# Kernel optimization log

Measured on AMD Instinct MI355X. Metric: run time of the kernel, lower is better.

## Reference

```python
import jax, jax.numpy as jnp
import numpy as np


def log_g(x):
    # Appendix B.3 of 'Were RNNs All We Needed?'
    return jnp.where(x >= 0, jnp.log(jax.nn.relu(x) + 0.5), -jax.nn.softplus(-x))


def parallel_scan_log(log_a, log_b):
    # h[0] = b[0]; h[i] = a[i]*h[i-1] + b[i], computed in log space along axis 1
    log_a_star = jnp.cumsum(log_a, axis=1)
    log_x0_plus_b_star = jax.lax.cumlogsumexp(log_b - log_a_star, axis=1)
    return jnp.exp(log_a_star + log_x0_plus_b_star)


def setup_inputs() -> dict:
    key = jax.random.key(0)
    B, T, D = 8, 4096, 1024
    k1, k2, k3, k4, k5 = jax.random.split(key, 5)
    scale = 1.0 / np.sqrt(D)
    return {
        "h_prev_layer": jax.random.normal(k1, (B, T, D), dtype=jnp.float32),
        "W_z": jax.random.uniform(k2, (D, D), jnp.float32, -scale, scale),
        "b_z": jax.random.uniform(k3, (D,), jnp.float32, -scale, scale),
        "W_h": jax.random.uniform(k4, (D, D), jnp.float32, -scale, scale),
        "b_h": jax.random.uniform(k5, (D,), jnp.float32, -scale, scale),
    }


def reference(h_prev_layer, W_z, b_z, W_h, b_h):
    k = jnp.einsum('btd,ed->bte', h_prev_layer, W_z) + b_z          # linear_z
    tilde_h = jnp.einsum('btd,ed->bte', h_prev_layer, W_h) + b_h    # linear_h
    log_z = -jax.nn.softplus(-k)
    log_one_minus_z = -jax.nn.softplus(k)
    log_tilde_h = log_g(tilde_h)
    return parallel_scan_log(log_one_minus_z, log_z + log_tilde_h)
```

## Files before the change

kernel.cpp:

```cpp
#include <hip/hip_runtime.h>
#include <hip/hip_fp16.h>

typedef float f32x4 __attribute__((ext_vector_type(4)));
typedef __bf16 bf16x8 __attribute__((ext_vector_type(8)));

#define BB_ 8
#define TT_ 4096
#define DD_ 1024
#define MM_ (BB_*TT_)
#define KK_ DD_

#define NCH 64
#define LCH (TT_/NCH)

static __device__ __forceinline__ unsigned short f2bf_rn(float f) {
  unsigned int u = __float_as_uint(f);
  u += 0x7FFFu + ((u >> 16) & 1u);
  return (unsigned short)(u >> 16);
}

__global__ void cvt_f32_bf16(const float4* __restrict__ src,
                             ushort4* __restrict__ dst, int n4) {
  int stride = gridDim.x * blockDim.x;
  for (int i = blockIdx.x * blockDim.x + threadIdx.x; i < n4; i += stride) {
    float4 v = src[i];
    ushort4 o;
    o.x = f2bf_rn(v.x); o.y = f2bf_rn(v.y);
    o.z = f2bf_rn(v.z); o.w = f2bf_rn(v.w);
    dst[i] = o;
  }
}

__global__ void cvt_w(const float4* __restrict__ Wz4,
                      const float4* __restrict__ Wh4,
                      ushort4* __restrict__ Wcat) {
  int flat = blockIdx.x * 256 + threadIdx.x;
  int mtx = flat >> 18;
  int j = flat & 262143;
  float4 v = (mtx ? Wh4 : Wz4)[j];
  int D = j >> 8;
  int kq = j & 255;
  int e = ((D >> 5) << 6) + (mtx << 5) + (D & 31);
  ushort4 o;
  o.x = f2bf_rn(v.x); o.y = f2bf_rn(v.y);
  o.z = f2bf_rn(v.z); o.w = f2bf_rn(v.w);
  Wcat[(size_t)e * 256 + kq] = o;
}

__device__ __forceinline__ void gload_lds16(const void* g, void* l) {
  __builtin_amdgcn_global_load_lds(
      (const __attribute__((address_space(1))) void*)g,
      (__attribute__((address_space(3))) void*)l, 16, 0, 0);
}

#define STA(q, nb_, kkh) gload_lds16(pXa + (q) * 65536 + (kkh), (nb_) + (q) * 8192 + wofs)
#define STB(q, nb_, kkh) gload_lds16(pWb + (q) * 65536 + (kkh), (nb_) + 32768 + (q) * 8192 + wofs)

#define PHASE(cb_, mh, kh, STAGEOPS, WAITOPS) do {                          \
    const char* Ab_ = (cb_);                                                \
    const char* Bb_ = (cb_) + 32768;                                        \
    const int sk_ = (kh) ? sk1 : sk0;                                       \
    bf16x8 af_[4];                                                          \
    _Pragma("unroll")                                                       \
    for (int ii = 0; ii < 4; ++ii)                                          \
      af_[ii] = *reinterpret_cast<const bf16x8*>(                           \
          Ab_ + rA7 + (mh) * 8192 + ii * 2048 + sk_);                       \
    if ((mh) == 0) {                                                        \
      _Pragma("unroll")                                                     \
      for (int j = 0; j < 4; ++j)                                           \
        bfv[j] = *reinterpret_cast<const bf16x8*>(                          \
            Bb_ + rB7 + j * 2048 + sk_);                                    \
    }                                                                       \
    STAGEOPS;                                                               \
    WAITOPS;                                                                \
    __builtin_amdgcn_s_barrier();                                           \
    asm volatile("s_waitcnt lgkmcnt(0)" ::: "memory");                      \
    __builtin_amdgcn_sched_barrier(0);                                      \
    __builtin_amdgcn_s_setprio(1);                                          \
    _Pragma("unroll")                                                       \
    for (int ii = 0; ii < 4; ++ii)                                          \
      _Pragma("unroll")                                                     \
      for (int j = 0; j < 4; ++j)                                           \
        acc[(mh) * 4 + ii][j] = __builtin_amdgcn_mfma_f32_16x16x32_bf16(    \
            af_[ii], bfv[j], acc[(mh) * 4 + ii][j], 0, 0, 0);               \
    __builtin_amdgcn_s_setprio(0);                                          \
    asm volatile("" ::: "memory");                                          \
    __builtin_amdgcn_s_barrier();                                           \
  } while (0)

__global__ __launch_bounds__(512, 2) void gemm_fused(
    const unsigned short* __restrict__ Xb,
    const unsigned short* __restrict__ Wb,
    const float* __restrict__ bz, const float* __restrict__ bh,
    unsigned int* __restrict__ ZG,
    float* __restrict__ Pp, float* __restrict__ Qq)
{
  extern __shared__ __align__(16) char smem[];
  const int tid  = threadIdx.x;
  const int wave = tid >> 6;
  const int lane = tid & 63;
  const int wm = wave >> 2, wn = wave & 3;
  const int fr = lane & 15, kg = lane >> 4;

  int swz = (blockIdx.x & 7) * 128 + (blockIdx.x >> 3);
  const int m0 = (swz >> 3) * 256;
  const int e0 = (swz & 7) * 256;

  const int arow = tid >> 3;
  const int aslx = ((tid & 7) ^ (arow & 7)) * 8;
  const unsigned short* pXa = Xb + (size_t)(m0 + arow) * KK_ + aslx;
  const unsigned short* pWb = Wb + (size_t)(e0 + arow) * KK_ + aslx;
  const int wofs = wave * 1024;

  const int rA7 = (wm * 128 + fr) * 128;
  const int rB7 = (wn * 64 + fr) * 128;
  const int fx = fr & 7;
  const int sk0 = (kg ^ fx) * 16;
  const int sk1 = sk0 ^ 64;

  f32x4 acc[8][4];
  #pragma unroll
  for (int i = 0; i < 8; i++)
    #pragma unroll
    for (int j = 0; j < 4; j++)
      acc[i][j] = (f32x4){0.f, 0.f, 0.f, 0.f};
  bf16x8 bfv[4];

  STA(0, smem, 0); STA(2, smem, 0); STB(0, smem, 0);
  STB(1, smem, 0); STB(2, smem, 0); STB(3, smem, 0);
  STA(1, smem, 0); STA(3, smem, 0);
  asm volatile("s_waitcnt vmcnt(2)" ::: "memory");
  __builtin_amdgcn_s_barrier();

  #pragma unroll 1
  for (int t = 0; t < 15; ++t) {
    char* cb = smem + ((t & 1) << 16);
    char* nb = smem + (((t + 1) & 1) << 16);
    const int kn = (t + 1) * 64;
    PHASE(cb, 0, 0, {STA(0, nb, kn); STA(2, nb, kn); STB(0, nb, kn);},
          asm volatile("s_waitcnt vmcnt(3)" ::: "memory"));
    PHASE(cb, 1, 0, {STB(1, nb, kn); STB(2, nb, kn); STB(3, nb, kn);}, );
    PHASE(cb, 0, 1, {STA(1, nb, kn); STA(3, nb, kn);}, );
    PHASE(cb, 1, 1, {},
          asm volatile("s_waitcnt vmcnt(2)" ::: "memory"));
  }
  {
    char* cb = smem + 65536;
    PHASE(cb, 0, 0, {}, asm volatile("s_waitcnt vmcnt(0)" ::: "memory"));
    PHASE(cb, 1, 0, {}, );
    PHASE(cb, 0, 1, {}, );
    PHASE(cb, 1, 1, {}, );
  }

  const int dw0 = (swz & 7) * 128 + wn * 32;
  const int t0 = m0 & 4095;
  const int bidx = m0 >> 12;

  float bzv[2], bhv[2];
  #pragma unroll
  for (int j = 0; j < 2; ++j) {
    bzv[j] = bz[dw0 + j * 16 + fr];
    bhv[j] = bh[dw0 + j * 16 + fr];
  }

  unsigned int* ew = (unsigned int*)(smem + wave * 9216);
  const int sub = lane & 7, rowr = lane >> 3;

  #pragma unroll
  for (int p = 0; p < 2; ++p) {
    float PP[2] = {1.f, 1.f}, QQ[2] = {0.f, 0.f};
    #pragma unroll
    for (int ii = 0; ii < 4; ++ii) {
      #pragma unroll
      for (int j = 0; j < 2; ++j) {
        float segP = 1.f, segQ = 0.f;
        #pragma unroll
        for (int r = 0; r < 4; ++r) {
          float kz = acc[p * 4 + ii][j][r] + bzv[j];
          float th = acc[p * 4 + ii][j + 2][r] + bhv[j];
          float z = 1.0f / (1.0f + __expf(-kz));
          float g = (th >= 0.0f) ? (th + 0.5f)
                                 : (1.0f / (1.0f + __expf(-th)));
          unsigned int pk =
              (unsigned int)__half_as_ushort(__float2half(z)) |
              ((unsigned int)__half_as_ushort(__float2half(g)) << 16);
          ew[(ii * 16 + kg * 4 + r) * 36 + j * 16 + fr] = pk;
          float aa = 1.f - z;
          segP *= aa;
          segQ = fmaf(aa, segQ, z * g);
        }
        float p1 = __shfl_down(segP, 16), q1 = __shfl_down(segQ, 16);
        segQ = fmaf(p1, segQ, q1); segP *= p1;
        float p2 = __shfl_down(segP, 32), q2 = __shfl_down(segQ, 32);
        segQ = fmaf(p2, segQ, q2); segP *= p2;
        QQ[j] = fmaf(segP, QQ[j], segQ);
        PP[j] *= segP;
      }
    }
    if (kg == 0) {
      const int cg = (t0 >> 6) + wm * 2 + p;
      #pragma unroll
      for (int j = 0; j < 2; ++j) {
        size_t po = ((size_t)bidx * NCH + cg) * DD_ + dw0 + j * 16 + fr;
        Pp[po] = PP[j];
        Qq[po] = QQ[j];
      }
    }
    #pragma unroll
    for (int q = 0; q < 8; ++q) {
      int rl = q * 8 + rowr;
      uint4 v = *reinterpret_cast<const uint4*>(&ew[rl * 36 + sub * 4]);
      size_t rg = (size_t)(m0 + wm * 128 + p * 64 + rl);
      *reinterpret_cast<uint4*>(&ZG[rg * DD_ + dw0 + sub * 4]) = v;
    }
  }
}

__global__ __launch_bounds__(256) void scan_combine(
    const float* __restrict__ P, const float* __restrict__ Q,
    float* __restrict__ H) {
  const int d = blockIdx.x * 256 + threadIdx.x;
  const int b = blockIdx.y;
  float h = 0.f;
  for (int c = 0; c < NCH; ++c) {
    size_t o = ((size_t)b * NCH + c) * DD_ + d;
    H[o] = h;
    h = fmaf(P[o], h, Q[o]);
  }
}

__global__ __launch_bounds__(256) void scan_apply(
    const uint4* __restrict__ ZG, const float4* __restrict__ H,
    float4* __restrict__ out) {
  const int d4 = threadIdx.x;
  const int c  = blockIdx.x;
  const int b  = blockIdx.y;
  float4 h = H[((size_t)b * NCH + c) * (DD_ / 4) + d4];
  size_t base = ((size_t)b * TT_ + (size_t)c * LCH) * (DD_ / 4) + d4;
  for (int t = 0; t < LCH; ++t) {
    uint4 w = ZG[base + (size_t)t * (DD_ / 4)];
    float z, g, a;
    z = __half2float(__ushort_as_half((unsigned short)(w.x & 0xffff)));
    g = __half2float(__ushort_as_half((unsigned short)(w.x >> 16)));
    a = 1.f - z; h.x = fmaf(a, h.x, z * g);
    z = __half2float(__ushort_as_half((unsigned short)(w.y & 0xffff)));
    g = __half2float(__ushort_as_half((unsigned short)(w.y >> 16)));
    a = 1.f - z; h.y = fmaf(a, h.y, z * g);
    z = __half2float(__ushort_as_half((unsigned short)(w.z & 0xffff)));
    g = __half2float(__ushort_as_half((unsigned short)(w.z >> 16)));
    a = 1.f - z; h.z = fmaf(a, h.z, z * g);
    z = __half2float(__ushort_as_half((unsigned short)(w.w & 0xffff)));
    g = __half2float(__ushort_as_half((unsigned short)(w.w >> 16)));
    a = 1.f - z; h.w = fmaf(a, h.w, z * g);
    out[base + (size_t)t * (DD_ / 4)] = h;
  }
}

extern "C" void kernel_launch(void* const* d_in, const int* in_sizes, int n_in,
                              void* d_out, int out_size, void* d_ws, size_t ws_size,
                              hipStream_t stream) {
  const float* X  = (const float*)d_in[0];
  const float* Wz = (const float*)d_in[1];
  const float* bz = (const float*)d_in[2];
  const float* Wh = (const float*)d_in[3];
  const float* bh = (const float*)d_in[4];
  float* out = (float*)d_out;

  const size_t szXb = (size_t)MM_ * DD_ * 2;
  const size_t szWb = (size_t)2 * DD_ * DD_ * 2;
  const size_t szZG = (size_t)MM_ * DD_ * 4;
  const size_t szPQ = (size_t)BB_ * NCH * DD_ * 4;

  char* ws = (char*)d_ws;
  unsigned short *Xb, *Wb;
  const size_t needA = szXb + szWb + szZG + 3 * szPQ;
  if (ws_size >= needA) {
    Xb = (unsigned short*)ws;              ws += szXb;
    Wb = (unsigned short*)ws;              ws += szWb;
  } else {
    Xb = (unsigned short*)d_out;
    Wb = (unsigned short*)((char*)d_out + szXb);
  }
  unsigned int* ZG = (unsigned int*)ws;  ws += szZG;
  float* P = (float*)ws;  ws += szPQ;
  float* Q = (float*)ws;  ws += szPQ;
  float* H = (float*)ws;

  cvt_f32_bf16<<<2048, 256, 0, stream>>>((const float4*)X, (ushort4*)Xb,
                                         (int)((size_t)MM_ * DD_ / 4));
  cvt_w<<<2048, 256, 0, stream>>>((const float4*)Wz, (const float4*)Wh,
                                  (ushort4*)Wb);
  gemm_fused<<<(MM_ / 256) * ((2 * DD_) / 256), 512, 131072, stream>>>(
      Xb, Wb, bz, bh, ZG, P, Q);

  scan_combine<<<dim3(4, BB_), 256, 0, stream>>>(P, Q, H);
  scan_apply<<<dim3(NCH, BB_), 256, 0, stream>>>((const uint4*)ZG,
                                                 (const float4*)H, (float4*)out);
}
```

Before: 264.1 us.

## Shrink GEMM tile to 128x256 with 4 waves and BK=32 double buffering

Restructures the fused GEMM from 256x256 tiles with 8 waves and K-step 64 (128 KB LDS) to 128x256 tiles with 4 waves, K-step 32 and 48 KB LDS. The LDS swizzle, staging layout and epilogue pass structure are reworked to match. The aim is more resident blocks per CU and better latency hiding. The cost is more K iterations, more barriers, and less data reuse per tile, which raises global traffic for the B matrix.

```diff
diff --git a/kernel.cpp b/kernel.cpp
--- a/kernel.cpp
+++ b/kernel.cpp
@@ -53,23 +53,20 @@
       (__attribute__((address_space(3))) void*)l, 16, 0, 0);
 }
 
-#define STA(q, nb_, kkh) gload_lds16(pXa + (q) * 65536 + (kkh), (nb_) + (q) * 8192 + wofs)
-#define STB(q, nb_, kkh) gload_lds16(pWb + (q) * 65536 + (kkh), (nb_) + 32768 + (q) * 8192 + wofs)
-
-#define PHASE(cb_, mh, kh, STAGEOPS, WAITOPS) do {                          \
-    const char* Ab_ = (cb_);                                                \
-    const char* Bb_ = (cb_) + 32768;                                        \
-    const int sk_ = (kh) ? sk1 : sk0;                                       \
+#define STA(q, nb_, kkh) gload_lds16(pXa + (q) * 65536 + (kkh), (nb_) + (q) * 4096 + wofs)
+#define STB(q, nb_, kkh) gload_lds16(pWb + (q) * 65536 + (kkh), (nb_) + 8192 + (q) * 4096 + wofs)
+
+#define PH(cb_, mh, STAGEOPS, WAITOPS) do {                                 \
+    const char* Ab_ = (const char*)(cb_);                                   \
     bf16x8 af_[4];                                                          \
     _Pragma("unroll")                                                       \
     for (int ii = 0; ii < 4; ++ii)                                          \
       af_[ii] = *reinterpret_cast<const bf16x8*>(                           \
-          Ab_ + rA7 + (mh) * 8192 + ii * 2048 + sk_);                       \
+          Ab_ + rAb + (mh) * 4096 + ii * 1024);                             \
     if ((mh) == 0) {                                                        \
       _Pragma("unroll")                                                     \
       for (int j = 0; j < 4; ++j)                                           \
-        bfv[j] = *reinterpret_cast<const bf16x8*>(                          \
-            Bb_ + rB7 + j * 2048 + sk_);                                    \
+        bfv[j] = *reinterpret_cast<const bf16x8*>(Ab_ + rBb + j * 1024);    \
     }                                                                       \
     STAGEOPS;                                                               \
     WAITOPS;                                                                \
@@ -88,7 +85,9 @@
     __builtin_amdgcn_s_barrier();                                           \
   } while (0)
 
-__global__ __launch_bounds__(512, 2) void gemm_fused(
+#define VMW(n) asm volatile("s_waitcnt vmcnt(" #n ")" ::: "memory")
+
+__global__ __launch_bounds__(256, 2) void gemm_fused(
     const unsigned short* __restrict__ Xb,
     const unsigned short* __restrict__ Wb,
     const float* __restrict__ bz, const float* __restrict__ bh,
@@ -99,24 +98,22 @@
   const int tid  = threadIdx.x;
   const int wave = tid >> 6;
   const int lane = tid & 63;
-  const int wm = wave >> 2, wn = wave & 3;
+  const int wn = wave;
   const int fr = lane & 15, kg = lane >> 4;
 
-  int swz = (blockIdx.x & 7) * 128 + (blockIdx.x >> 3);
-  const int m0 = (swz >> 3) * 256;
+  int swz = (blockIdx.x & 7) * 256 + (blockIdx.x >> 3);
+  const int m0 = (swz >> 3) * 128;
   const int e0 = (swz & 7) * 256;
 
-  const int arow = tid >> 3;
-  const int aslx = ((tid & 7) ^ (arow & 7)) * 8;
-  const unsigned short* pXa = Xb + (size_t)(m0 + arow) * KK_ + aslx;
-  const unsigned short* pWb = Wb + (size_t)(e0 + arow) * KK_ + aslx;
+  const int rr = tid >> 2;
+  const int ac = ((tid & 3) ^ (rr & 3)) * 8;
+  const unsigned short* pXa = Xb + (size_t)(m0 + rr) * KK_ + ac;
+  const unsigned short* pWb = Wb + (size_t)(e0 + rr) * KK_ + ac;
   const int wofs = wave * 1024;
 
-  const int rA7 = (wm * 128 + fr) * 128;
-  const int rB7 = (wn * 64 + fr) * 128;
-  const int fx = fr & 7;
-  const int sk0 = (kg ^ fx) * 16;
-  const int sk1 = sk0 ^ 64;
+  const int cksw = ((kg ^ (fr & 3)) << 4);
+  const int rAb = fr * 64 + cksw;
+  const int rBb = 8192 + (wn * 64 + fr) * 64 + cksw;
 
   f32x4 acc[8][4];
   #pragma unroll
@@ -126,30 +123,25 @@
       acc[i][j] = (f32x4){0.f, 0.f, 0.f, 0.f};
   bf16x8 bfv[4];
 
-  STA(0, smem, 0); STA(2, smem, 0); STB(0, smem, 0);
-  STB(1, smem, 0); STB(2, smem, 0); STB(3, smem, 0);
-  STA(1, smem, 0); STA(3, smem, 0);
-  asm volatile("s_waitcnt vmcnt(2)" ::: "memory");
+  STA(0, smem, 0); STA(1, smem, 0);
+  STB(0, smem, 0); STB(1, smem, 0); STB(2, smem, 0); STB(3, smem, 0);
+  VMW(0);
   __builtin_amdgcn_s_barrier();
 
   #pragma unroll 1
-  for (int t = 0; t < 15; ++t) {
-    char* cb = smem + ((t & 1) << 16);
-    char* nb = smem + (((t + 1) & 1) << 16);
-    const int kn = (t + 1) * 64;
-    PHASE(cb, 0, 0, {STA(0, nb, kn); STA(2, nb, kn); STB(0, nb, kn);},
-          asm volatile("s_waitcnt vmcnt(3)" ::: "memory"));
-    PHASE(cb, 1, 0, {STB(1, nb, kn); STB(2, nb, kn); STB(3, nb, kn);}, );
-    PHASE(cb, 0, 1, {STA(1, nb, kn); STA(3, nb, kn);}, );
-    PHASE(cb, 1, 1, {},
-          asm volatile("s_waitcnt vmcnt(2)" ::: "memory"));
+  for (int t = 0; t < 31; ++t) {
+    const char* cb = smem + (t & 1) * 24576;
+    char* nb = smem + ((t + 1) & 1) * 24576;
+    const int kn = (t + 1) * 32;
+    PH(cb, 0, {STA(0, nb, kn); STA(1, nb, kn);
+               STB(0, nb, kn); STB(1, nb, kn);
+               STB(2, nb, kn); STB(3, nb, kn);}, );
+    PH(cb, 1, {}, VMW(0));
   }
   {
-    char* cb = smem + 65536;
-    PHASE(cb, 0, 0, {}, asm volatile("s_waitcnt vmcnt(0)" ::: "memory"));
-    PHASE(cb, 1, 0, {}, );
-    PHASE(cb, 0, 1, {}, );
-    PHASE(cb, 1, 1, {}, );
+    const char* cb = smem + 24576;
+    PH(cb, 0, {}, );
+    PH(cb, 1, {}, );
   }
 
   const int dw0 = (swz & 7) * 128 + wn * 32;
@@ -163,28 +155,30 @@
     bhv[j] = bh[dw0 + j * 16 + fr];
   }
 
-  unsigned int* ew = (unsigned int*)(smem + wave * 9216);
+  unsigned int* ew = (unsigned int*)(smem + wave * 4608);
   const int sub = lane & 7, rowr = lane >> 3;
 
+  float PP[2], QQ[2];
   #pragma unroll
-  for (int p = 0; p < 2; ++p) {
-    float PP[2] = {1.f, 1.f}, QQ[2] = {0.f, 0.f};
+  for (int pass = 0; pass < 4; ++pass) {
+    if ((pass & 1) == 0) { PP[0] = PP[1] = 1.f; QQ[0] = QQ[1] = 0.f; }
     #pragma unroll
-    for (int ii = 0; ii < 4; ++ii) {
+    for (int iil = 0; iil < 2; ++iil) {
+      const int ii = pass * 2 + iil;
       #pragma unroll
       for (int j = 0; j < 2; ++j) {
         float segP = 1.f, segQ = 0.f;
         #pragma unroll
         for (int r = 0; r < 4; ++r) {
-          float kz = acc[p * 4 + ii][j][r] + bzv[j];
-          float th = acc[p * 4 + ii][j + 2][r] + bhv[j];
+          float kz = acc[ii][j][r] + bzv[j];
+          float th = acc[ii][j + 2][r] + bhv[j];
           float z = 1.0f / (1.0f + __expf(-kz));
           float g = (th >= 0.0f) ? (th + 0.5f)
                                  : (1.0f / (1.0f + __expf(-th)));
           unsigned int pk =
               (unsigned int)__half_as_ushort(__float2half(z)) |
               ((unsigned int)__half_as_ushort(__float2half(g)) << 16);
-          ew[(ii * 16 + kg * 4 + r) * 36 + j * 16 + fr] = pk;
+          ew[(iil * 16 + kg * 4 + r) * 36 + j * 16 + fr] = pk;
           float aa = 1.f - z;
           segP *= aa;
           segQ = fmaf(aa, segQ, z * g);
@@ -197,8 +191,8 @@
         PP[j] *= segP;
       }
     }
-    if (kg == 0) {
-      const int cg = (t0 >> 6) + wm * 2 + p;
+    if ((pass & 1) == 1 && kg == 0) {
+      const int cg = (t0 >> 6) + (pass >> 1);
       #pragma unroll
       for (int j = 0; j < 2; ++j) {
         size_t po = ((size_t)bidx * NCH + cg) * DD_ + dw0 + j * 16 + fr;
@@ -207,10 +201,10 @@
       }
     }
     #pragma unroll
-    for (int q = 0; q < 8; ++q) {
+    for (int q = 0; q < 4; ++q) {
       int rl = q * 8 + rowr;
       uint4 v = *reinterpret_cast<const uint4*>(&ew[rl * 36 + sub * 4]);
-      size_t rg = (size_t)(m0 + wm * 128 + p * 64 + rl);
+      size_t rg = (size_t)(m0 + pass * 32 + rl);
       *reinterpret_cast<uint4*>(&ZG[rg * DD_ + dw0 + sub * 4]) = v;
     }
   }
@@ -290,7 +284,7 @@
                                          (int)((size_t)MM_ * DD_ / 4));
   cvt_w<<<2048, 256, 0, stream>>>((const float4*)Wz, (const float4*)Wh,
                                   (ushort4*)Wb);
-  gemm_fused<<<(MM_ / 256) * ((2 * DD_) / 256), 512, 131072, stream>>>(
+  gemm_fused<<<(MM_ / 128) * ((2 * DD_) / 256), 256, 49152, stream>>>(
       Xb, Wb, bz, bh, ZG, P, Q);
 
   scan_combine<<<dim3(4, BB_), 256, 0, stream>>>(P, Q, H);
```

After: 274.0 us. 1.04x slower.

## Fuse scan into GEMM with decoupled look-back across time tiles

Applied to the files above, without the earlier changes.

Folds the chunk-combine and scan-apply kernels into the GEMM kernel. Each block keeps its z/g values in LDS, publishes its chunk aggregate with a release flag, and looks back over up to 15 earlier blocks of the same batch sequence to get its carry-in, then writes the final output directly. This removes the global ZG intermediate round trip and two extra launches. In exchange, LDS use rises to about 134 KB, occupancy drops to one block per CU, and blocks now spin on global flags, which depends on earlier blocks being scheduled first and has a bounded-spin fallback that could give wrong results.

```diff
diff --git a/kernel.cpp b/kernel.cpp
--- a/kernel.cpp
+++ b/kernel.cpp
@@ -10,13 +10,17 @@
 #define MM_ (BB_*TT_)
 #define KK_ DD_
 
-#define NCH 64
-#define LCH (TT_/NCH)
-
 static __device__ __forceinline__ unsigned short f2bf_rn(float f) {
   unsigned int u = __float_as_uint(f);
   u += 0x7FFFu + ((u >> 16) & 1u);
   return (unsigned short)(u >> 16);
+}
+
+static __device__ __forceinline__ int ld_acq(const int* p) {
+  return __hip_atomic_load(p, __ATOMIC_ACQUIRE, __HIP_MEMORY_SCOPE_AGENT);
+}
+static __device__ __forceinline__ void st_rel(int* p, int v) {
+  __hip_atomic_store(p, v, __ATOMIC_RELEASE, __HIP_MEMORY_SCOPE_AGENT);
 }
 
 __global__ void cvt_f32_bf16(const float4* __restrict__ src,
@@ -88,23 +92,31 @@
     __builtin_amdgcn_s_barrier();                                           \
   } while (0)
 
-__global__ __launch_bounds__(512, 2) void gemm_fused(
+__global__ __launch_bounds__(512, 1) void gemm_scan(
     const unsigned short* __restrict__ Xb,
     const unsigned short* __restrict__ Wb,
     const float* __restrict__ bz, const float* __restrict__ bh,
-    unsigned int* __restrict__ ZG,
-    float* __restrict__ Pp, float* __restrict__ Qq)
+    float2* __restrict__ aggG,
+    int* __restrict__ flagG,
+    float* __restrict__ out)
 {
   extern __shared__ __align__(16) char smem[];
+  unsigned int* zgL = (unsigned int*)smem;
+  float2* pqL = (float2*)(smem + 131072);
+  float* harr = (float*)(smem + 135168);
+
   const int tid  = threadIdx.x;
   const int wave = tid >> 6;
   const int lane = tid & 63;
   const int wm = wave >> 2, wn = wave & 3;
   const int fr = lane & 15, kg = lane >> 4;
 
-  int swz = (blockIdx.x & 7) * 128 + (blockIdx.x >> 3);
-  const int m0 = (swz >> 3) * 256;
-  const int e0 = (swz & 7) * 256;
+  const int bid = blockIdx.x;
+  const int nq = bid >> 7;
+  const int mglob = bid & 127;
+  const int m0 = mglob * 256;
+  const int e0 = nq * 256;
+  const int chainpos = mglob & 15;
 
   const int arow = tid >> 3;
   const int aslx = ((tid & 7) ^ (arow & 7)) * 8;
@@ -152,19 +164,13 @@
     PHASE(cb, 1, 1, {}, );
   }
 
-  const int dw0 = (swz & 7) * 128 + wn * 32;
-  const int t0 = m0 & 4095;
-  const int bidx = m0 >> 12;
-
+  const int chl = wn * 32;
   float bzv[2], bhv[2];
   #pragma unroll
   for (int j = 0; j < 2; ++j) {
-    bzv[j] = bz[dw0 + j * 16 + fr];
-    bhv[j] = bh[dw0 + j * 16 + fr];
-  }
-
-  unsigned int* ew = (unsigned int*)(smem + wave * 9216);
-  const int sub = lane & 7, rowr = lane >> 3;
+    bzv[j] = bz[nq * 128 + chl + j * 16 + fr];
+    bhv[j] = bh[nq * 128 + chl + j * 16 + fr];
+  }
 
   #pragma unroll
   for (int p = 0; p < 2; ++p) {
@@ -176,15 +182,15 @@
         float segP = 1.f, segQ = 0.f;
         #pragma unroll
         for (int r = 0; r < 4; ++r) {
+          const int t = wm * 128 + p * 64 + ii * 16 + kg * 4 + r;
           float kz = acc[p * 4 + ii][j][r] + bzv[j];
           float th = acc[p * 4 + ii][j + 2][r] + bhv[j];
           float z = 1.0f / (1.0f + __expf(-kz));
           float g = (th >= 0.0f) ? (th + 0.5f)
                                  : (1.0f / (1.0f + __expf(-th)));
-          unsigned int pk =
+          zgL[t * 128 + chl + j * 16 + fr] =
               (unsigned int)__half_as_ushort(__float2half(z)) |
               ((unsigned int)__half_as_ushort(__float2half(g)) << 16);
-          ew[(ii * 16 + kg * 4 + r) * 36 + j * 16 + fr] = pk;
           float aa = 1.f - z;
           segP *= aa;
           segQ = fmaf(aa, segQ, z * g);
@@ -198,61 +204,62 @@
       }
     }
     if (kg == 0) {
-      const int cg = (t0 >> 6) + wm * 2 + p;
       #pragma unroll
-      for (int j = 0; j < 2; ++j) {
-        size_t po = ((size_t)bidx * NCH + cg) * DD_ + dw0 + j * 16 + fr;
-        Pp[po] = PP[j];
-        Qq[po] = QQ[j];
+      for (int j = 0; j < 2; ++j)
+        pqL[(wm * 2 + p) * 128 + chl + j * 16 + fr] = make_float2(PP[j], QQ[j]);
+    }
+  }
+  __syncthreads();
+
+  float cP[4], cQ[4], bP = 1.f, bQ = 0.f;
+  if (tid < 128) {
+    #pragma unroll
+    for (int k = 0; k < 4; ++k) {
+      float2 c = pqL[k * 128 + tid];
+      cP[k] = c.x; cQ[k] = c.y;
+      bQ = fmaf(c.x, bQ, c.y);
+      bP *= c.x;
+    }
+    aggG[(size_t)bid * 128 + tid] = make_float2(bP, bQ);
+    __threadfence();
+  }
+  __syncthreads();
+  if (tid == 0) st_rel(&flagG[bid], 1);
+
+  if (tid < 128) {
+    float accP = 1.f, accQ = 0.f;
+    const int stop = bid - chainpos;
+    for (int j = bid - 1; j >= stop; --j) {
+      int spins = 0;
+      while (ld_acq(&flagG[j]) == 0) {
+        __builtin_amdgcn_s_sleep(8);
+        if (++spins > (1 << 24)) break;
       }
-    }
-    #pragma unroll
-    for (int q = 0; q < 8; ++q) {
-      int rl = q * 8 + rowr;
-      uint4 v = *reinterpret_cast<const uint4*>(&ew[rl * 36 + sub * 4]);
-      size_t rg = (size_t)(m0 + wm * 128 + p * 64 + rl);
-      *reinterpret_cast<uint4*>(&ZG[rg * DD_ + dw0 + sub * 4]) = v;
-    }
-  }
-}
-
-__global__ __launch_bounds__(256) void scan_combine(
-    const float* __restrict__ P, const float* __restrict__ Q,
-    float* __restrict__ H) {
-  const int d = blockIdx.x * 256 + threadIdx.x;
-  const int b = blockIdx.y;
-  float h = 0.f;
-  for (int c = 0; c < NCH; ++c) {
-    size_t o = ((size_t)b * NCH + c) * DD_ + d;
-    H[o] = h;
-    h = fmaf(P[o], h, Q[o]);
-  }
-}
-
-__global__ __launch_bounds__(256) void scan_apply(
-    const uint4* __restrict__ ZG, const float4* __restrict__ H,
-    float4* __restrict__ out) {
-  const int d4 = threadIdx.x;
-  const int c  = blockIdx.x;
-  const int b  = blockIdx.y;
-  float4 h = H[((size_t)b * NCH + c) * (DD_ / 4) + d4];
-  size_t base = ((size_t)b * TT_ + (size_t)c * LCH) * (DD_ / 4) + d4;
-  for (int t = 0; t < LCH; ++t) {
-    uint4 w = ZG[base + (size_t)t * (DD_ / 4)];
-    float z, g, a;
-    z = __half2float(__ushort_as_half((unsigned short)(w.x & 0xffff)));
-    g = __half2float(__ushort_as_half((unsigned short)(w.x >> 16)));
-    a = 1.f - z; h.x = fmaf(a, h.x, z * g);
-    z = __half2float(__ushort_as_half((unsigned short)(w.y & 0xffff)));
-    g = __half2float(__ushort_as_half((unsigned short)(w.y >> 16)));
-    a = 1.f - z; h.y = fmaf(a, h.y, z * g);
-    z = __half2float(__ushort_as_half((unsigned short)(w.z & 0xffff)));
-    g = __half2float(__ushort_as_half((unsigned short)(w.z >> 16)));
-    a = 1.f - z; h.z = fmaf(a, h.z, z * g);
-    z = __half2float(__ushort_as_half((unsigned short)(w.w & 0xffff)));
-    g = __half2float(__ushort_as_half((unsigned short)(w.w >> 16)));
-    a = 1.f - z; h.w = fmaf(a, h.w, z * g);
-    out[base + (size_t)t * (DD_ / 4)] = h;
+      float2 a = aggG[(size_t)j * 128 + tid];
+      accQ = fmaf(accP, a.y, accQ);
+      accP *= a.x;
+    }
+    float h = accQ;
+    #pragma unroll
+    for (int k = 0; k < 4; ++k) {
+      harr[k * 128 + tid] = h;
+      h = fmaf(cP[k], h, cQ[k]);
+    }
+  }
+  __syncthreads();
+
+  {
+    const int ch = tid & 127, q = tid >> 7;
+    float h = harr[q * 128 + ch];
+    float* op = out + (size_t)(m0 + q * 64) * DD_ + nq * 128 + ch;
+    #pragma unroll 4
+    for (int i = 0; i < 64; ++i) {
+      unsigned int w = zgL[(q * 64 + i) * 128 + ch];
+      float z = __half2float(__ushort_as_half((unsigned short)(w & 0xffff)));
+      float g = __half2float(__ushort_as_half((unsigned short)(w >> 16)));
+      h = fmaf(1.f - z, h, z * g);
+      op[(size_t)i * DD_] = h;
+    }
   }
 }
 
@@ -268,32 +275,20 @@
 
   const size_t szXb = (size_t)MM_ * DD_ * 2;
   const size_t szWb = (size_t)2 * DD_ * DD_ * 2;
-  const size_t szZG = (size_t)MM_ * DD_ * 4;
-  const size_t szPQ = (size_t)BB_ * NCH * DD_ * 4;
+  const size_t szAg = (size_t)1024 * 128 * 8;
+  const size_t szFl = 1024 * sizeof(int);
 
   char* ws = (char*)d_ws;
-  unsigned short *Xb, *Wb;
-  const size_t needA = szXb + szWb + szZG + 3 * szPQ;
-  if (ws_size >= needA) {
-    Xb = (unsigned short*)ws;              ws += szXb;
-    Wb = (unsigned short*)ws;              ws += szWb;
-  } else {
-    Xb = (unsigned short*)d_out;
-    Wb = (unsigned short*)((char*)d_out + szXb);
-  }
-  unsigned int* ZG = (unsigned int*)ws;  ws += szZG;
-  float* P = (float*)ws;  ws += szPQ;
-  float* Q = (float*)ws;  ws += szPQ;
-  float* H = (float*)ws;
+  unsigned short* Xb = (unsigned short*)ws;  ws += szXb;
+  unsigned short* Wb = (unsigned short*)ws;  ws += szWb;
+  float2* aggG = (float2*)ws;                ws += szAg;
+  int* flagG = (int*)ws;                     ws += szFl;
+
+  hipMemsetAsync(flagG, 0, szFl, stream);
 
   cvt_f32_bf16<<<2048, 256, 0, stream>>>((const float4*)X, (ushort4*)Xb,
                                          (int)((size_t)MM_ * DD_ / 4));
   cvt_w<<<2048, 256, 0, stream>>>((const float4*)Wz, (const float4*)Wh,
                                   (ushort4*)Wb);
-  gemm_fused<<<(MM_ / 256) * ((2 * DD_) / 256), 512, 131072, stream>>>(
-      Xb, Wb, bz, bh, ZG, P, Q);
-
-  scan_combine<<<dim3(4, BB_), 256, 0, stream>>>(P, Q, H);
-  scan_apply<<<dim3(NCH, BB_), 256, 0, stream>>>((const uint4*)ZG,
-                                                 (const float4*)H, (float4*)out);
-}
+  gemm_scan<<<1024, 512, 137216, stream>>>(Xb, Wb, bz, bh, aggG, flagG, out);
+}
```

After: 409.5 us. 1.55x slower.

## Software-pipeline LDS fragment reads one phase ahead of MFMA in GEMM loop

Applied to the files above, without the earlier changes.

Restructures the GEMM main loop so the LDS reads for the next phase are issued, as inline-asm ds_read_b128 into alternating register sets, before the current phase's MFMAs run. Partial lgkmcnt waits replace the full waits, and one barrier per phase replaces two. The aim is to hide LDS read latency behind matrix-core work and cut synchronisation stalls. In exchange it needs more registers and relies on hand-tuned wait counts, which could cost occupancy or correctness if a count is wrong.

```diff
diff --git a/kernel.cpp b/kernel.cpp
--- a/kernel.cpp
+++ b/kernel.cpp
@@ -3,6 +3,8 @@
 
 typedef float f32x4 __attribute__((ext_vector_type(4)));
 typedef __bf16 bf16x8 __attribute__((ext_vector_type(8)));
+typedef unsigned int u32x4 __attribute__((ext_vector_type(4)));
+typedef __attribute__((address_space(3))) const void* lds_cp;
 
 #define BB_ 8
 #define TT_ 4096
@@ -56,37 +58,40 @@
 #define STA(q, nb_, kkh) gload_lds16(pXa + (q) * 65536 + (kkh), (nb_) + (q) * 8192 + wofs)
 #define STB(q, nb_, kkh) gload_lds16(pWb + (q) * 65536 + (kkh), (nb_) + 32768 + (q) * 8192 + wofs)
 
-#define PHASE(cb_, mh, kh, STAGEOPS, WAITOPS) do {                          \
-    const char* Ab_ = (cb_);                                                \
-    const char* Bb_ = (cb_) + 32768;                                        \
-    const int sk_ = (kh) ? sk1 : sk0;                                       \
-    bf16x8 af_[4];                                                          \
-    _Pragma("unroll")                                                       \
-    for (int ii = 0; ii < 4; ++ii)                                          \
-      af_[ii] = *reinterpret_cast<const bf16x8*>(                           \
-          Ab_ + rA7 + (mh) * 8192 + ii * 2048 + sk_);                       \
-    if ((mh) == 0) {                                                        \
-      _Pragma("unroll")                                                     \
-      for (int j = 0; j < 4; ++j)                                           \
-        bfv[j] = *reinterpret_cast<const bf16x8*>(                          \
-            Bb_ + rB7 + j * 2048 + sk_);                                    \
-    }                                                                       \
-    STAGEOPS;                                                               \
-    WAITOPS;                                                                \
-    __builtin_amdgcn_s_barrier();                                           \
-    asm volatile("s_waitcnt lgkmcnt(0)" ::: "memory");                      \
-    __builtin_amdgcn_sched_barrier(0);                                      \
+#define DSR(dst, gp) \
+  asm volatile("ds_read_b128 %0, %1" : "=&v"(dst) : "v"((lds_cp)(gp)))
+
+#define RD_A(SET, base_, mh, sk_) do {                                      \
+    DSR(SET[0], (base_) + rA7 + (mh) * 8192 + 0 * 2048 + (sk_));            \
+    DSR(SET[1], (base_) + rA7 + (mh) * 8192 + 1 * 2048 + (sk_));            \
+    DSR(SET[2], (base_) + rA7 + (mh) * 8192 + 2 * 2048 + (sk_));            \
+    DSR(SET[3], (base_) + rA7 + (mh) * 8192 + 3 * 2048 + (sk_));            \
+  } while (0)
+#define RD_B(SET, base_, sk_) do {                                          \
+    DSR(SET[0], (base_) + rB7 + 0 * 2048 + (sk_));                          \
+    DSR(SET[1], (base_) + rB7 + 1 * 2048 + (sk_));                          \
+    DSR(SET[2], (base_) + rB7 + 2 * 2048 + (sk_));                          \
+    DSR(SET[3], (base_) + rB7 + 3 * 2048 + (sk_));                          \
+  } while (0)
+
+#define BC(x) __builtin_bit_cast(bf16x8, x)
+#define MFMA16(ASET, BSET, mh) do {                                         \
     __builtin_amdgcn_s_setprio(1);                                          \
     _Pragma("unroll")                                                       \
     for (int ii = 0; ii < 4; ++ii)                                          \
       _Pragma("unroll")                                                     \
       for (int j = 0; j < 4; ++j)                                           \
         acc[(mh) * 4 + ii][j] = __builtin_amdgcn_mfma_f32_16x16x32_bf16(    \
-            af_[ii], bfv[j], acc[(mh) * 4 + ii][j], 0, 0, 0);               \
+            BC(ASET[ii]), BC(BSET[j]), acc[(mh) * 4 + ii][j], 0, 0, 0);     \
     __builtin_amdgcn_s_setprio(0);                                          \
-    asm volatile("" ::: "memory");                                          \
-    __builtin_amdgcn_s_barrier();                                           \
   } while (0)
+
+#define BAR() do { __builtin_amdgcn_s_barrier();                            \
+                   __builtin_amdgcn_sched_barrier(0); } while (0)
+#define SB()  __builtin_amdgcn_sched_barrier(0)
+#define LGKM(n) do { asm volatile("s_waitcnt lgkmcnt(" #n ")" ::: "memory");\
+                     SB(); } while (0)
+#define VMW(n) asm volatile("s_waitcnt vmcnt(" #n ")" ::: "memory")
 
 __global__ __launch_bounds__(512, 2) void gemm_fused(
     const unsigned short* __restrict__ Xb,
@@ -113,7 +118,7 @@
   const int wofs = wave * 1024;
 
   const int rA7 = (wm * 128 + fr) * 128;
-  const int rB7 = (wn * 64 + fr) * 128;
+  const int rB7 = 32768 + (wn * 64 + fr) * 128;
   const int fx = fr & 7;
   const int sk0 = (kg ^ fx) * 16;
   const int sk1 = sk0 ^ 64;
@@ -124,33 +129,63 @@
     #pragma unroll
     for (int j = 0; j < 4; j++)
       acc[i][j] = (f32x4){0.f, 0.f, 0.f, 0.f};
-  bf16x8 bfv[4];
+  u32x4 aP[4], aQ[4], bk0[4], bk1[4];
 
   STA(0, smem, 0); STA(2, smem, 0); STB(0, smem, 0);
   STB(1, smem, 0); STB(2, smem, 0); STB(3, smem, 0);
   STA(1, smem, 0); STA(3, smem, 0);
-  asm volatile("s_waitcnt vmcnt(2)" ::: "memory");
+  VMW(2);
   __builtin_amdgcn_s_barrier();
+  SB();
+  RD_A(aP, smem, 0, sk0);
+  RD_B(bk0, smem, sk0);
 
   #pragma unroll 1
   for (int t = 0; t < 15; ++t) {
-    char* cb = smem + ((t & 1) << 16);
+    const char* cb = smem + ((t & 1) << 16);
     char* nb = smem + (((t + 1) & 1) << 16);
     const int kn = (t + 1) * 64;
-    PHASE(cb, 0, 0, {STA(0, nb, kn); STA(2, nb, kn); STB(0, nb, kn);},
-          asm volatile("s_waitcnt vmcnt(3)" ::: "memory"));
-    PHASE(cb, 1, 0, {STB(1, nb, kn); STB(2, nb, kn); STB(3, nb, kn);}, );
-    PHASE(cb, 0, 1, {STA(1, nb, kn); STA(3, nb, kn);}, );
-    PHASE(cb, 1, 1, {},
-          asm volatile("s_waitcnt vmcnt(2)" ::: "memory"));
+    VMW(0);
+    BAR();
+    RD_A(aQ, cb, 1, sk0);
+    STA(0, nb, kn); STA(2, nb, kn); STB(0, nb, kn);
+    LGKM(4);
+    MFMA16(aP, bk0, 0);
+    BAR();
+    RD_A(aP, cb, 0, sk1);
+    RD_B(bk1, cb, sk1);
+    STB(1, nb, kn); STB(2, nb, kn); STB(3, nb, kn);
+    LGKM(8);
+    MFMA16(aQ, bk0, 1);
+    BAR();
+    RD_A(aQ, cb, 1, sk1);
+    STA(1, nb, kn); STA(3, nb, kn);
+    LGKM(4);
+    MFMA16(aP, bk1, 0);
+    VMW(2);
+    BAR();
+    RD_A(aP, nb, 0, sk0);
+    RD_B(bk0, nb, sk0);
+    LGKM(8);
+    MFMA16(aQ, bk1, 1);
   }
   {
-    char* cb = smem + 65536;
-    PHASE(cb, 0, 0, {}, asm volatile("s_waitcnt vmcnt(0)" ::: "memory"));
-    PHASE(cb, 1, 0, {}, );
-    PHASE(cb, 0, 1, {}, );
-    PHASE(cb, 1, 1, {}, );
-  }
+    const char* cb = smem + 65536;
+    VMW(0);
+    BAR();
+    RD_A(aQ, cb, 1, sk0);
+    LGKM(4);  MFMA16(aP, bk0, 0);
+    BAR();
+    RD_A(aP, cb, 0, sk1);
+    RD_B(bk1, cb, sk1);
+    LGKM(8);  MFMA16(aQ, bk0, 1);
+    BAR();
+    RD_A(aQ, cb, 1, sk1);
+    LGKM(4);  MFMA16(aP, bk1, 0);
+    BAR();
+    LGKM(0);  MFMA16(aQ, bk1, 1);
+  }
+  __syncthreads();
 
   const int dw0 = (swz & 7) * 128 + wn * 32;
   const int t0 = m0 & 4095;
```

Measured after the change: 263.4 us. About the same (-0.3%).
